# Performance work log

Hardware: AMD Instinct MI355X
Metric: run time of the kernel (lower is better)

The kernel has to match this reference:

```python
import jax, jax.numpy as jnp
import numpy as np

GROUPS = 32
EPS = 1e-5
HEADS = 8

def setup_inputs() -> dict:
    key = jax.random.key(0)
    ks = jax.random.split(key, 7)
    b, c, H, W = 16, 512, 32, 32
    x = jax.random.normal(ks[0], (b, c, H, W), dtype=jnp.float32)
    gn_scale = jax.random.normal(ks[1], (c,), dtype=jnp.float32) * 0.02 + 1.0
    gn_bias = jax.random.normal(ks[2], (c,), dtype=jnp.float32) * 0.02
    w_qkv = jax.random.normal(ks[3], (3 * c, c), dtype=jnp.float32) / np.sqrt(c)
    b_qkv = jax.random.normal(ks[4], (3 * c,), dtype=jnp.float32) * 0.01
    # original zero-initializes proj_out; use random weights for a non-trivial baseline
    w_proj = jax.random.normal(ks[5], (c, c), dtype=jnp.float32) / np.sqrt(c)
    b_proj = jax.random.normal(ks[6], (c,), dtype=jnp.float32) * 0.01
    return {"x": x, "gn_scale": gn_scale, "gn_bias": gn_bias,
            "w_qkv": w_qkv, "b_qkv": b_qkv, "w_proj": w_proj, "b_proj": b_proj}

def _group_norm(x, scale, bias):
    # x: [b, c, T]; normalize over (c//GROUPS, T) per group
    b, c, T = x.shape
    xg = x.reshape(b, GROUPS, (c // GROUPS) * T)
    mean = xg.mean(axis=-1, keepdims=True)
    var = xg.var(axis=-1, keepdims=True)
    xn = ((xg - mean) * jax.lax.rsqrt(var + EPS)).reshape(b, c, T)
    return xn * scale[None, :, None] + bias[None, :, None]

def reference(x, gn_scale, gn_bias, w_qkv, b_qkv, w_proj, b_proj):
    b, c, H, W = x.shape
    T = H * W
    xf = x.reshape(b, c, T)
    h = _group_norm(xf, gn_scale, gn_bias)
    qkv = jnp.einsum('oc,bct->bot', w_qkv, h) + b_qkv[None, :, None]  # [b, 3c, T]
    qkv = qkv.reshape(b * HEADS, 3 * (c // HEADS), T)
    ch = c // HEADS
    q, k, v = jnp.split(qkv, 3, axis=1)  # each [b*heads, ch, T]
    scale = 1.0 / np.sqrt(np.sqrt(ch))
    weight = jnp.einsum('bct,bcs->bts', q * scale, k * scale)  # [b*heads, T, T]
    weight = jax.nn.softmax(weight.astype(jnp.float32), axis=-1).astype(qkv.dtype)
    r = jnp.einsum('bts,bcs->bct', weight, v)  # [b*heads, ch, T]
    r = r.reshape(b, c, T)
    out = jnp.einsum('oc,bct->bot', w_proj, r) + b_proj[None, :, None]
    return (xf + out).reshape(b, c, H, W)
```

## Files before the change

kernel.cpp:

```cpp
#include <hip/hip_runtime.h>
#include <stdint.h>
#include <stddef.h>

#define NB 16
#define NC 512
#define NT 1024
#define NHEAD 8
#define NOC 1536

typedef float f32x4 __attribute__((ext_vector_type(4)));
typedef short s16x8 __attribute__((ext_vector_type(8)));
typedef short s16x4 __attribute__((ext_vector_type(4)));
typedef unsigned int u32x2 __attribute__((ext_vector_type(2)));

#define AS1 __attribute__((address_space(1)))
#define AS3 __attribute__((address_space(3)))

static __device__ __forceinline__ unsigned short f2bf(float f) {
  union { float fv; unsigned int u; } v; v.fv = f;
  return (unsigned short)((v.u + 0x7fffu + ((v.u >> 16) & 1u)) >> 16);
}

static __device__ __forceinline__ unsigned int cvtpk(float lo, float hi) {
  unsigned int r;
  asm("v_cvt_pk_bf16_f32 %0, %1, %2" : "=v"(r) : "v"(lo), "v"(hi));
  return r;
}

static __device__ __forceinline__ float exp2_hw(float x) {
  float r;
  asm("v_exp_f32 %0, %1" : "=v"(r) : "v"(x));
  return r;
}

__global__ void k_convert(const float* __restrict__ wq, const float* __restrict__ wp,
                          unsigned short* __restrict__ wqb, unsigned short* __restrict__ wpb) {
  int i = blockIdx.x * 256 + threadIdx.x;
  int step = gridDim.x * 256;
  for (int idx = i; idx < NOC * NC; idx += step) wqb[idx] = f2bf(wq[idx]);
  for (int idx = i; idx < NC * NC; idx += step) wpb[idx] = f2bf(wp[idx]);
}

__global__ __launch_bounds__(256) void k_gnstats(const float* __restrict__ x,
    const float* __restrict__ gsc, const float* __restrict__ gbi,
    float* __restrict__ affA, float* __restrict__ affB) {
  int b = blockIdx.x >> 5, g = blockIdx.x & 31;
  const f32x4* p4 = (const f32x4*)(x + (size_t)(b * NC + g * 16) * NT);
  float s = 0.f, ss = 0.f;
  for (int i = threadIdx.x; i < 4096; i += 256) {
    f32x4 v = p4[i];
    s += v[0] + v[1] + v[2] + v[3];
    ss += v[0] * v[0] + v[1] * v[1] + v[2] * v[2] + v[3] * v[3];
  }
#pragma unroll
  for (int off = 32; off > 0; off >>= 1) { s += __shfl_down(s, off); ss += __shfl_down(ss, off); }
  __shared__ float red[4][2];
  if ((threadIdx.x & 63) == 0) { red[threadIdx.x >> 6][0] = s; red[threadIdx.x >> 6][1] = ss; }
  __syncthreads();
  if (threadIdx.x < 16) {
    float st = red[0][0] + red[1][0] + red[2][0] + red[3][0];
    float sst = red[0][1] + red[1][1] + red[2][1] + red[3][1];
    float mean = st * (1.f / 16384.f);
    float var = sst * (1.f / 16384.f) - mean * mean;
    float rstd = rsqrtf(var + 1e-5f);
    int c = g * 16 + threadIdx.x;
    float a = rstd * gsc[c];
    affA[b * NC + c] = a;
    affB[b * NC + c] = gbi[c] - mean * a;
  }
}

__global__ __launch_bounds__(256) void k_norm_t(const float* __restrict__ x,
    const float* __restrict__ affA, const float* __restrict__ affB,
    unsigned short* __restrict__ xt) {
  __shared__ float sm[64][65];
  int bx = blockIdx.x;
  int tt = bx & 15, ct = (bx >> 4) & 7, b = bx >> 7;
  int c0 = ct * 64, t0 = tt * 64;
  int tid = threadIdx.x;
#pragma unroll
  for (int it = 0; it < 4; it++) {
    int row = (tid >> 4) + it * 16;
    int col = (tid & 15) * 4;
    int c = c0 + row;
    f32x4 v = *(const f32x4*)(x + (size_t)(b * NC + c) * NT + t0 + col);
    float a = affA[b * NC + c], bb = affB[b * NC + c];
    sm[row][col + 0] = v[0] * a + bb;
    sm[row][col + 1] = v[1] * a + bb;
    sm[row][col + 2] = v[2] * a + bb;
    sm[row][col + 3] = v[3] * a + bb;
  }
  __syncthreads();
#pragma unroll
  for (int it = 0; it < 2; it++) {
    int t = (tid >> 3) + it * 32;
    int cb = (tid & 7) * 8;
    s16x8 o;
#pragma unroll
    for (int j = 0; j < 8; j++) o[j] = (short)f2bf(sm[cb + j][t]);
    *(s16x8*)(xt + (size_t)(b * NT + t0 + t) * NC + c0 + cb) = o;
  }
}

__global__ __launch_bounds__(256) void k_qkv(const unsigned short* __restrict__ wqb,
    const unsigned short* __restrict__ xt, const float* __restrict__ bqkv,
    unsigned short* __restrict__ qt, unsigned short* __restrict__ ktb,
    unsigned short* __restrict__ vvb) {
  __shared__ char Al[8192];
  __shared__ char Bl[8192];
  __shared__ char Tr[4][8192];
  int n0 = blockIdx.x * 128;
  int m0 = blockIdx.y * 128;
  int b = blockIdx.z;
  int tid = threadIdx.x, lane = tid & 63, wid = tid >> 6;
  int wr = wid >> 1, wc = wid & 1;
  int arow = lane >> 2, acol = (lane & 3) * 8;
  f32x4 acc[4][4] = {};
  for (int ks = 0; ks < 16; ks++) {
    int k0 = ks * 32;
    __syncthreads();
#pragma unroll
    for (int cc = 0; cc < 2; cc++) {
      int ci = wid * 2 + cc;
      const unsigned short* ga = wqb + (size_t)(m0 + ci * 16 + arow) * NC + k0 + acol;
      __builtin_amdgcn_global_load_lds((const AS1 unsigned int*)ga,
                                       (AS3 unsigned int*)(Al + ci * 1024), 16, 0, 0);
      const unsigned short* gb = xt + (size_t)(b * NT + n0 + ci * 16 + arow) * NC + k0 + acol;
      __builtin_amdgcn_global_load_lds((const AS1 unsigned int*)gb,
                                       (AS3 unsigned int*)(Bl + ci * 1024), 16, 0, 0);
    }
    __syncthreads();
    s16x8 af[4], bfv[4];
#pragma unroll
    for (int mi = 0; mi < 4; mi++)
      af[mi] = *(const s16x8*)(Al + ((wr * 64 + mi * 16 + (lane & 15)) * 32 + (lane >> 4) * 8) * 2);
#pragma unroll
    for (int ni = 0; ni < 4; ni++)
      bfv[ni] = *(const s16x8*)(Bl + ((wc * 64 + ni * 16 + (lane & 15)) * 32 + (lane >> 4) * 8) * 2);
#pragma unroll
    for (int mi = 0; mi < 4; mi++)
#pragma unroll
      for (int ni = 0; ni < 4; ni++)
        acc[mi][ni] = __builtin_amdgcn_mfma_f32_16x16x32_bf16(af[mi], bfv[ni], acc[mi][ni], 0, 0, 0);
  }
  char* tr = (char*)Tr[wid];
  int o064 = m0 + wr * 64;
  int blk = (o064 >> 6) % 3;
  int head = o064 / 192;
  int bh = b * NHEAD + head;
  int n0w = n0 + wc * 64;
  const float scale = 0.42466090014400953f;
  if (blk < 2) {
#pragma unroll
    for (int mi = 0; mi < 4; mi++) {
      int o_loc = mi * 16 + (lane >> 4) * 4;
      float b0 = bqkv[o064 + o_loc + 0], b1 = bqkv[o064 + o_loc + 1];
      float b2 = bqkv[o064 + o_loc + 2], b3 = bqkv[o064 + o_loc + 3];
#pragma unroll
      for (int ni = 0; ni < 4; ni++) {
        int t_loc = ni * 16 + (lane & 15);
        s16x4 pk;
        pk[0] = (short)f2bf((acc[mi][ni][0] + b0) * scale);
        pk[1] = (short)f2bf((acc[mi][ni][1] + b1) * scale);
        pk[2] = (short)f2bf((acc[mi][ni][2] + b2) * scale);
        pk[3] = (short)f2bf((acc[mi][ni][3] + b3) * scale);
        *(s16x4*)(tr + t_loc * 128 + ((o_loc * 2) ^ ((t_loc & 7) << 4))) = pk;
      }
    }
    unsigned short* outp = (blk == 0) ? qt : ktb;
#pragma unroll
    for (int pass = 0; pass < 8; pass++) {
      int t = pass * 8 + (lane >> 3);
      int cb = (lane & 7) * 16;
      s16x8 v = *(const s16x8*)(tr + t * 128 + (cb ^ ((t & 7) << 4)));
      *(s16x8*)(outp + (size_t)(bh * NT + n0w + t) * 64 + (cb >> 1)) = v;
    }
  } else {
#pragma unroll
    for (int mi = 0; mi < 4; mi++) {
#pragma unroll
      for (int ni = 0; ni < 4; ni++) {
        int t_loc = ni * 16 + (lane & 15);
#pragma unroll
        for (int r = 0; r < 4; r++) {
          int o_loc = mi * 16 + (lane >> 4) * 4 + r;
          *(unsigned short*)(tr + o_loc * 128 + t_loc * 2) =
              f2bf(acc[mi][ni][r] + bqkv[o064 + o_loc]);
        }
      }
    }
#pragma unroll
    for (int pass = 0; pass < 8; pass++) {
      int o = pass * 8 + (lane >> 3);
      int tb = (lane & 7) * 16;
      s16x8 v = *(const s16x8*)(tr + o * 128 + tb);
      *(s16x8*)(vvb + (size_t)(bh * 64 + o) * NT + n0w + (tb >> 1)) = v;
    }
  }
}

__global__ __launch_bounds__(512, 4) void k_attn(const unsigned short* __restrict__ qt,
    const unsigned short* __restrict__ ktb, const unsigned short* __restrict__ vvb,
    unsigned short* __restrict__ rt) {
  __shared__ char Kl[2][8192];
  __shared__ char Vl[2][8192];
  __shared__ char Pl[8][4096];
  int qt0 = blockIdx.x * 256;
  int bh = blockIdx.y;
  int b = bh >> 3, head = bh & 7;
  int tid = threadIdx.x, lane = tid & 63, wid = tid >> 6;
  int hi = lane >> 4, lo = lane & 15;
  int q0 = qt0 + wid * 32;
  s16x8 aq[2][2];
#pragma unroll
  for (int mi = 0; mi < 2; mi++)
#pragma unroll
    for (int ko = 0; ko < 2; ko++)
      aq[mi][ko] = *(const s16x8*)(qt + (size_t)(bh * NT + q0 + mi * 16 + lo) * 64 +
                                   ko * 32 + hi * 8);
  f32x4 oacc[2][4] = {};
  f32x4 lacc[2] = {};
  float mrun[2] = {-1e30f, -1e30f};
  s16x8 ones;
#pragma unroll
  for (int j = 0; j < 8; j++) ones[j] = (short)0x3F80;
  char* pl = (char*)Pl[wid];
  int srow = (wid << 3) + (lane >> 3);
  int soff = ((lane & 7) << 4) ^ ((srow & 7) << 4);
  const char* kb = (const char*)ktb + ((size_t)bh * NT + srow) * 128 + soff;
  const char* vb = (const char*)vvb + ((size_t)(bh * 64 + srow)) * 2048 + soff;
  __builtin_amdgcn_global_load_lds((const AS1 unsigned int*)kb,
                                   (AS3 unsigned int*)(Kl[0] + (wid << 10)), 16, 0, 0);
  __builtin_amdgcn_global_load_lds((const AS1 unsigned int*)vb,
                                   (AS3 unsigned int*)(Vl[0] + (wid << 10)), 16, 0, 0);
  for (int kv = 0; kv < 16; kv++) {
    int cur = kv & 1;
    if (kv < 15) {
      __builtin_amdgcn_global_load_lds((const AS1 unsigned int*)(kb + (size_t)(kv + 1) * 8192),
                                       (AS3 unsigned int*)(Kl[cur ^ 1] + (wid << 10)), 16, 0, 0);
      __builtin_amdgcn_global_load_lds((const AS1 unsigned int*)(vb + (size_t)(kv + 1) * 128),
                                       (AS3 unsigned int*)(Vl[cur ^ 1] + (wid << 10)), 16, 0, 0);
      asm volatile("s_waitcnt vmcnt(2)" ::: "memory");
    } else {
      asm volatile("s_waitcnt vmcnt(0)" ::: "memory");
    }
    __builtin_amdgcn_s_barrier();
    __builtin_amdgcn_sched_barrier(0);
    f32x4 sc[2][4] = {};
#pragma unroll
    for (int ni = 0; ni < 4; ni++) {
      int tkr = ni * 16 + lo;
#pragma unroll
      for (int ko = 0; ko < 2; ko++) {
        s16x8 kf = *(const s16x8*)(Kl[cur] + tkr * 128 + ((ko * 64 + hi * 16) ^ ((tkr & 7) << 4)));
        sc[0][ni] = __builtin_amdgcn_mfma_f32_16x16x32_bf16(kf, aq[0][ko], sc[0][ni], 0, 0, 0);
        sc[1][ni] = __builtin_amdgcn_mfma_f32_16x16x32_bf16(kf, aq[1][ko], sc[1][ni], 0, 0, 0);
      }
    }
#pragma unroll
    for (int mi = 0; mi < 2; mi++) {
      float a0 = fmaxf(fmaxf(sc[mi][0][0], sc[mi][0][1]), fmaxf(sc[mi][0][2], sc[mi][0][3]));
      float a1 = fmaxf(fmaxf(sc[mi][1][0], sc[mi][1][1]), fmaxf(sc[mi][1][2], sc[mi][1][3]));
      float a2 = fmaxf(fmaxf(sc[mi][2][0], sc[mi][2][1]), fmaxf(sc[mi][2][2], sc[mi][2][3]));
      float a3 = fmaxf(fmaxf(sc[mi][3][0], sc[mi][3][1]), fmaxf(sc[mi][3][2], sc[mi][3][3]));
      float tm = fmaxf(fmaxf(a0, a1), fmaxf(a2, a3));
      tm = fmaxf(tm, __shfl_xor(tm, 16));
      tm = fmaxf(tm, __shfl_xor(tm, 32));
      int resc = __any(tm > mrun[mi] + 8.f);
      float mnew = mrun[mi];
      if (resc) {
        mnew = fmaxf(mrun[mi], tm);
        float fac = exp2_hw(mrun[mi] - mnew);
        mrun[mi] = mnew;
#pragma unroll
        for (int dm = 0; dm < 4; dm++)
#pragma unroll
          for (int r = 0; r < 4; r++) oacc[mi][dm][r] *= fac;
#pragma unroll
        for (int r = 0; r < 4; r++) lacc[mi][r] *= fac;
      }
#pragma unroll
      for (int ni = 0; ni < 4; ni++)
#pragma unroll
        for (int r = 0; r < 4; r++) sc[mi][ni][r] = exp2_hw(sc[mi][ni][r] - mnew);
      int qrow = mi * 16 + lo;
#pragma unroll
      for (int ni = 0; ni < 4; ni++) {
        u32x2 w;
        w[0] = cvtpk(sc[mi][ni][0], sc[mi][ni][1]);
        w[1] = cvtpk(sc[mi][ni][2], sc[mi][ni][3]);
        *(u32x2*)(pl + (qrow * 128 + ((ni * 32 + hi * 8) ^ ((qrow & 7) << 4)))) = w;
      }
    }
#pragma unroll
    for (int kt = 0; kt < 2; kt++) {
      s16x8 pa[2];
#pragma unroll
      for (int mi = 0; mi < 2; mi++) {
        int qrow = mi * 16 + lo;
        pa[mi] = *(const s16x8*)(pl + (qrow * 128 + ((kt * 64 + hi * 16) ^ ((qrow & 7) << 4))));
      }
#pragma unroll
      for (int dm = 0; dm < 4; dm++) {
        int dr = dm * 16 + lo;
        s16x8 av = *(const s16x8*)(Vl[cur] + dr * 128 + ((kt * 64 + hi * 16) ^ ((dr & 7) << 4)));
        oacc[0][dm] = __builtin_amdgcn_mfma_f32_16x16x32_bf16(av, pa[0], oacc[0][dm], 0, 0, 0);
        oacc[1][dm] = __builtin_amdgcn_mfma_f32_16x16x32_bf16(av, pa[1], oacc[1][dm], 0, 0, 0);
      }
      lacc[0] = __builtin_amdgcn_mfma_f32_16x16x32_bf16(ones, pa[0], lacc[0], 0, 0, 0);
      lacc[1] = __builtin_amdgcn_mfma_f32_16x16x32_bf16(ones, pa[1], lacc[1], 0, 0, 0);
    }
    __builtin_amdgcn_s_barrier();
  }
#pragma unroll
  for (int mi = 0; mi < 2; mi++) {
    float inv = 1.f / lacc[mi][0];
    int q = q0 + mi * 16 + lo;
#pragma unroll
    for (int dm = 0; dm < 4; dm++) {
      u32x2 w;
      w[0] = cvtpk(oacc[mi][dm][0] * inv, oacc[mi][dm][1] * inv);
      w[1] = cvtpk(oacc[mi][dm][2] * inv, oacc[mi][dm][3] * inv);
      *(u32x2*)(rt + (size_t)(b * NT + q) * NC + head * 64 + dm * 16 + hi * 4) = w;
    }
  }
}

__global__ __launch_bounds__(256) void k_proj(const unsigned short* __restrict__ wpb,
    const unsigned short* __restrict__ rt, const float* __restrict__ bproj,
    const float* __restrict__ x, float* __restrict__ out) {
  __shared__ char Al[8192];
  __shared__ char Bl[8192];
  int n0 = blockIdx.x * 128;
  int m0 = blockIdx.y * 128;
  int b = blockIdx.z;
  int tid = threadIdx.x, lane = tid & 63, wid = tid >> 6;
  int wr = wid >> 1, wc = wid & 1;
  int arow = lane >> 2, acol = (lane & 3) * 8;
  f32x4 acc[4][4] = {};
  for (int ks = 0; ks < 16; ks++) {
    int k0 = ks * 32;
    __syncthreads();
#pragma unroll
    for (int cc = 0; cc < 2; cc++) {
      int ci = wid * 2 + cc;
      const unsigned short* ga = wpb + (size_t)(m0 + ci * 16 + arow) * NC + k0 + acol;
      __builtin_amdgcn_global_load_lds((const AS1 unsigned int*)ga,
                                       (AS3 unsigned int*)(Al + ci * 1024), 16, 0, 0);
      const unsigned short* gb = rt + (size_t)(b * NT + n0 + ci * 16 + arow) * NC + k0 + acol;
      __builtin_amdgcn_global_load_lds((const AS1 unsigned int*)gb,
                                       (AS3 unsigned int*)(Bl + ci * 1024), 16, 0, 0);
    }
    __syncthreads();
    s16x8 af[4], bfv[4];
#pragma unroll
    for (int mi = 0; mi < 4; mi++)
      af[mi] = *(const s16x8*)(Al + ((wr * 64 + mi * 16 + (lane & 15)) * 32 + (lane >> 4) * 8) * 2);
#pragma unroll
    for (int ni = 0; ni < 4; ni++)
      bfv[ni] = *(const s16x8*)(Bl + ((wc * 64 + ni * 16 + (lane & 15)) * 32 + (lane >> 4) * 8) * 2);
#pragma unroll
    for (int mi = 0; mi < 4; mi++)
#pragma unroll
      for (int ni = 0; ni < 4; ni++)
        acc[mi][ni] = __builtin_amdgcn_mfma_f32_16x16x32_bf16(af[mi], bfv[ni], acc[mi][ni], 0, 0, 0);
  }
#pragma unroll
  for (int mi = 0; mi < 4; mi++) {
    int o_base = m0 + wr * 64 + mi * 16 + (lane >> 4) * 4;
#pragma unroll
    for (int r = 0; r < 4; r++) {
      int o = o_base + r;
      float bp = bproj[o];
#pragma unroll
      for (int ni = 0; ni < 4; ni++) {
        int t = n0 + wc * 64 + ni * 16 + (lane & 15);
        size_t idx = (size_t)(b * NC + o) * NT + t;
        out[idx] = acc[mi][ni][r] + bp + x[idx];
      }
    }
  }
}

extern "C" void kernel_launch(void* const* d_in, const int* in_sizes, int n_in,
                              void* d_out, int out_size, void* d_ws, size_t ws_size,
                              hipStream_t stream) {
  const float* x   = (const float*)d_in[0];
  const float* gsc = (const float*)d_in[1];
  const float* gbi = (const float*)d_in[2];
  const float* wq  = (const float*)d_in[3];
  const float* bq  = (const float*)d_in[4];
  const float* wp  = (const float*)d_in[5];
  const float* bp  = (const float*)d_in[6];
  float* out = (float*)d_out;
  char* ws = (char*)d_ws;

  float* affA = (float*)ws;
  float* affB = affA + NB * NC;
  unsigned short* wqb = (unsigned short*)(ws + 65536);
  unsigned short* wpb = wqb + (size_t)NOC * NC;
  unsigned short* xt  = (unsigned short*)(ws + 2162688);
  unsigned short* qt  = xt + (size_t)NB * NT * NC;
  unsigned short* ktb = qt + (size_t)128 * NT * 64;
  unsigned short* vvb = ktb + (size_t)128 * NT * 64;
  unsigned short* rt  = vvb + (size_t)128 * NT * 64;

  k_convert<<<dim3(1024), 256, 0, stream>>>(wq, wp, wqb, wpb);
  k_gnstats<<<dim3(512), 256, 0, stream>>>(x, gsc, gbi, affA, affB);
  k_norm_t<<<dim3(2048), 256, 0, stream>>>(x, affA, affB, xt);
  k_qkv<<<dim3(8, 12, 16), 256, 0, stream>>>(wqb, xt, bq, qt, ktb, vvb);
  k_attn<<<dim3(4, 128), 512, 0, stream>>>(qt, ktb, vvb, rt);
  k_proj<<<dim3(8, 4, 16), 256, 0, stream>>>(wpb, rt, bp, x, out);
}
```

Baseline: 135.7 us.

## Double-buffer LDS tiles in QKV and projection GEMMs and raise MFMA priority

The QKV and output-projection GEMM kernels now prefetch the next K-slice into a second LDS buffer through global_load_lds while computing on the current one. This replaces the two __syncthreads per step with an explicit vmcnt wait and barrier. s_setprio is also raised around the MFMA blocks in the GEMMs and the attention kernel so matrix work is issued ahead of other waves. In QKV the transpose scratch now reuses the shared buffer, which keeps LDS at 32KB. The proj kernel's LDS grows from 16KB to 32KB, which may lower occupancy.

```diff
diff --git a/kernel.cpp b/kernel.cpp
--- a/kernel.cpp
+++ b/kernel.cpp
@@ -106,9 +106,7 @@
     const unsigned short* __restrict__ xt, const float* __restrict__ bqkv,
     unsigned short* __restrict__ qt, unsigned short* __restrict__ ktb,
     unsigned short* __restrict__ vvb) {
-  __shared__ char Al[8192];
-  __shared__ char Bl[8192];
-  __shared__ char Tr[4][8192];
+  __shared__ char LB[32768];
   int n0 = blockIdx.x * 128;
   int m0 = blockIdx.y * 128;
   int b = blockIdx.z;
@@ -116,34 +114,56 @@
   int wr = wid >> 1, wc = wid & 1;
   int arow = lane >> 2, acol = (lane & 3) * 8;
   f32x4 acc[4][4] = {};
+#pragma unroll
+  for (int cc = 0; cc < 2; cc++) {
+    int ci = wid * 2 + cc;
+    const unsigned short* ga = wqb + (size_t)(m0 + ci * 16 + arow) * NC + acol;
+    __builtin_amdgcn_global_load_lds((const AS1 unsigned int*)ga,
+                                     (AS3 unsigned int*)(LB + ci * 1024), 16, 0, 0);
+    const unsigned short* gb = xt + (size_t)(b * NT + n0 + ci * 16 + arow) * NC + acol;
+    __builtin_amdgcn_global_load_lds((const AS1 unsigned int*)gb,
+                                     (AS3 unsigned int*)(LB + 8192 + ci * 1024), 16, 0, 0);
+  }
   for (int ks = 0; ks < 16; ks++) {
-    int k0 = ks * 32;
-    __syncthreads();
-#pragma unroll
-    for (int cc = 0; cc < 2; cc++) {
-      int ci = wid * 2 + cc;
-      const unsigned short* ga = wqb + (size_t)(m0 + ci * 16 + arow) * NC + k0 + acol;
-      __builtin_amdgcn_global_load_lds((const AS1 unsigned int*)ga,
-                                       (AS3 unsigned int*)(Al + ci * 1024), 16, 0, 0);
-      const unsigned short* gb = xt + (size_t)(b * NT + n0 + ci * 16 + arow) * NC + k0 + acol;
-      __builtin_amdgcn_global_load_lds((const AS1 unsigned int*)gb,
-                                       (AS3 unsigned int*)(Bl + ci * 1024), 16, 0, 0);
-    }
-    __syncthreads();
+    int cur = ks & 1;
+    char* Ac = LB + cur * 16384;
+    char* Bc = Ac + 8192;
+    if (ks < 15) {
+      int k0n = (ks + 1) * 32;
+      char* An = LB + (cur ^ 1) * 16384;
+#pragma unroll
+      for (int cc = 0; cc < 2; cc++) {
+        int ci = wid * 2 + cc;
+        const unsigned short* ga = wqb + (size_t)(m0 + ci * 16 + arow) * NC + k0n + acol;
+        __builtin_amdgcn_global_load_lds((const AS1 unsigned int*)ga,
+                                         (AS3 unsigned int*)(An + ci * 1024), 16, 0, 0);
+        const unsigned short* gb = xt + (size_t)(b * NT + n0 + ci * 16 + arow) * NC + k0n + acol;
+        __builtin_amdgcn_global_load_lds((const AS1 unsigned int*)gb,
+                                         (AS3 unsigned int*)(An + 8192 + ci * 1024), 16, 0, 0);
+      }
+      asm volatile("s_waitcnt vmcnt(4)" ::: "memory");
+    } else {
+      asm volatile("s_waitcnt vmcnt(0)" ::: "memory");
+    }
+    __builtin_amdgcn_s_barrier();
+    __builtin_amdgcn_sched_barrier(0);
     s16x8 af[4], bfv[4];
 #pragma unroll
     for (int mi = 0; mi < 4; mi++)
-      af[mi] = *(const s16x8*)(Al + ((wr * 64 + mi * 16 + (lane & 15)) * 32 + (lane >> 4) * 8) * 2);
+      af[mi] = *(const s16x8*)(Ac + ((wr * 64 + mi * 16 + (lane & 15)) * 32 + (lane >> 4) * 8) * 2);
 #pragma unroll
     for (int ni = 0; ni < 4; ni++)
-      bfv[ni] = *(const s16x8*)(Bl + ((wc * 64 + ni * 16 + (lane & 15)) * 32 + (lane >> 4) * 8) * 2);
+      bfv[ni] = *(const s16x8*)(Bc + ((wc * 64 + ni * 16 + (lane & 15)) * 32 + (lane >> 4) * 8) * 2);
+    __builtin_amdgcn_s_setprio(1);
 #pragma unroll
     for (int mi = 0; mi < 4; mi++)
 #pragma unroll
       for (int ni = 0; ni < 4; ni++)
         acc[mi][ni] = __builtin_amdgcn_mfma_f32_16x16x32_bf16(af[mi], bfv[ni], acc[mi][ni], 0, 0, 0);
-  }
-  char* tr = (char*)Tr[wid];
+    __builtin_amdgcn_s_setprio(0);
+    __builtin_amdgcn_s_barrier();
+  }
+  char* tr = LB + wid * 8192;
   int o064 = m0 + wr * 64;
   int blk = (o064 >> 6) % 3;
   int head = o064 / 192;
@@ -247,6 +267,7 @@
     __builtin_amdgcn_s_barrier();
     __builtin_amdgcn_sched_barrier(0);
     f32x4 sc[2][4] = {};
+    __builtin_amdgcn_s_setprio(1);
 #pragma unroll
     for (int ni = 0; ni < 4; ni++) {
       int tkr = ni * 16 + lo;
@@ -257,6 +278,7 @@
         sc[1][ni] = __builtin_amdgcn_mfma_f32_16x16x32_bf16(kf, aq[1][ko], sc[1][ni], 0, 0, 0);
       }
     }
+    __builtin_amdgcn_s_setprio(0);
 #pragma unroll
     for (int mi = 0; mi < 2; mi++) {
       float a0 = fmaxf(fmaxf(sc[mi][0][0], sc[mi][0][1]), fmaxf(sc[mi][0][2], sc[mi][0][3]));
@@ -300,6 +322,7 @@
         int qrow = mi * 16 + lo;
         pa[mi] = *(const s16x8*)(pl + (qrow * 128 + ((kt * 64 + hi * 16) ^ ((qrow & 7) << 4))));
       }
+      __builtin_amdgcn_s_setprio(1);
 #pragma unroll
       for (int dm = 0; dm < 4; dm++) {
         int dr = dm * 16 + lo;
@@ -309,6 +332,7 @@
       }
       lacc[0] = __builtin_amdgcn_mfma_f32_16x16x32_bf16(ones, pa[0], lacc[0], 0, 0, 0);
       lacc[1] = __builtin_amdgcn_mfma_f32_16x16x32_bf16(ones, pa[1], lacc[1], 0, 0, 0);
+      __builtin_amdgcn_s_setprio(0);
     }
     __builtin_amdgcn_s_barrier();
   }
@@ -329,8 +353,7 @@
 __global__ __launch_bounds__(256) void k_proj(const unsigned short* __restrict__ wpb,
     const unsigned short* __restrict__ rt, const float* __restrict__ bproj,
     const float* __restrict__ x, float* __restrict__ out) {
-  __shared__ char Al[8192];
-  __shared__ char Bl[8192];
+  __shared__ char LB[32768];
   int n0 = blockIdx.x * 128;
   int m0 = blockIdx.y * 128;
   int b = blockIdx.z;
@@ -338,32 +361,54 @@
   int wr = wid >> 1, wc = wid & 1;
   int arow = lane >> 2, acol = (lane & 3) * 8;
   f32x4 acc[4][4] = {};
+#pragma unroll
+  for (int cc = 0; cc < 2; cc++) {
+    int ci = wid * 2 + cc;
+    const unsigned short* ga = wpb + (size_t)(m0 + ci * 16 + arow) * NC + acol;
+    __builtin_amdgcn_global_load_lds((const AS1 unsigned int*)ga,
+                                     (AS3 unsigned int*)(LB + ci * 1024), 16, 0, 0);
+    const unsigned short* gb = rt + (size_t)(b * NT + n0 + ci * 16 + arow) * NC + acol;
+    __builtin_amdgcn_global_load_lds((const AS1 unsigned int*)gb,
+                                     (AS3 unsigned int*)(LB + 8192 + ci * 1024), 16, 0, 0);
+  }
   for (int ks = 0; ks < 16; ks++) {
-    int k0 = ks * 32;
-    __syncthreads();
-#pragma unroll
-    for (int cc = 0; cc < 2; cc++) {
-      int ci = wid * 2 + cc;
-      const unsigned short* ga = wpb + (size_t)(m0 + ci * 16 + arow) * NC + k0 + acol;
-      __builtin_amdgcn_global_load_lds((const AS1 unsigned int*)ga,
-                                       (AS3 unsigned int*)(Al + ci * 1024), 16, 0, 0);
-      const unsigned short* gb = rt + (size_t)(b * NT + n0 + ci * 16 + arow) * NC + k0 + acol;
-      __builtin_amdgcn_global_load_lds((const AS1 unsigned int*)gb,
-                                       (AS3 unsigned int*)(Bl + ci * 1024), 16, 0, 0);
-    }
-    __syncthreads();
+    int cur = ks & 1;
+    char* Ac = LB + cur * 16384;
+    char* Bc = Ac + 8192;
+    if (ks < 15) {
+      int k0n = (ks + 1) * 32;
+      char* An = LB + (cur ^ 1) * 16384;
+#pragma unroll
+      for (int cc = 0; cc < 2; cc++) {
+        int ci = wid * 2 + cc;
+        const unsigned short* ga = wpb + (size_t)(m0 + ci * 16 + arow) * NC + k0n + acol;
+        __builtin_amdgcn_global_load_lds((const AS1 unsigned int*)ga,
+                                         (AS3 unsigned int*)(An + ci * 1024), 16, 0, 0);
+        const unsigned short* gb = rt + (size_t)(b * NT + n0 + ci * 16 + arow) * NC + k0n + acol;
+        __builtin_amdgcn_global_load_lds((const AS1 unsigned int*)gb,
+                                         (AS3 unsigned int*)(An + 8192 + ci * 1024), 16, 0, 0);
+      }
+      asm volatile("s_waitcnt vmcnt(4)" ::: "memory");
+    } else {
+      asm volatile("s_waitcnt vmcnt(0)" ::: "memory");
+    }
+    __builtin_amdgcn_s_barrier();
+    __builtin_amdgcn_sched_barrier(0);
     s16x8 af[4], bfv[4];
 #pragma unroll
     for (int mi = 0; mi < 4; mi++)
-      af[mi] = *(const s16x8*)(Al + ((wr * 64 + mi * 16 + (lane & 15)) * 32 + (lane >> 4) * 8) * 2);
+      af[mi] = *(const s16x8*)(Ac + ((wr * 64 + mi * 16 + (lane & 15)) * 32 + (lane >> 4) * 8) * 2);
 #pragma unroll
     for (int ni = 0; ni < 4; ni++)
-      bfv[ni] = *(const s16x8*)(Bl + ((wc * 64 + ni * 16 + (lane & 15)) * 32 + (lane >> 4) * 8) * 2);
+      bfv[ni] = *(const s16x8*)(Bc + ((wc * 64 + ni * 16 + (lane & 15)) * 32 + (lane >> 4) * 8) * 2);
+    __builtin_amdgcn_s_setprio(1);
 #pragma unroll
     for (int mi = 0; mi < 4; mi++)
 #pragma unroll
       for (int ni = 0; ni < 4; ni++)
         acc[mi][ni] = __builtin_amdgcn_mfma_f32_16x16x32_bf16(af[mi], bfv[ni], acc[mi][ni], 0, 0, 0);
+    __builtin_amdgcn_s_setprio(0);
+    __builtin_amdgcn_s_barrier();
   }
 #pragma unroll
   for (int mi = 0; mi < 4; mi++) {
```

After: 137.2 us. Within noise of the previous version (+1.1%).
